# Kernel tuning notes

Measured on AMD Instinct MI355X. Metric: run time of the kernel, lower is better.

Reference implementation:

```python
import jax, jax.numpy as jnp
import numpy as np

N_MODELS = 16
IN_F = 1024
OUT_F = 1024
N_TOK = 8192


def setup_inputs() -> dict:
    key = jax.random.key(0)
    k1, k2, k3, k4 = jax.random.split(key, 4)
    x = jax.random.normal(k1, (N_TOK, IN_F), dtype=jnp.float32)
    idxs = jax.random.randint(k2, (N_TOK,), 0, N_MODELS, dtype=jnp.int64)
    w = jax.random.normal(k3, (N_MODELS, IN_F, OUT_F), dtype=jnp.float32) * 0.02
    b = jax.random.normal(k4, (N_MODELS, OUT_F), dtype=jnp.float32) * 0.02
    return {"x": x, "idxs": idxs, "w": w, "b": b}


def reference(x, idxs, w, b):
    # Equivalent math to the torch loop: for each expert i, tokens with
    # idxs==i get x @ w[i] + b[i]; finally ReLU over all outputs.
    # Loop over the small fixed expert count; selection by mask avoids
    # materializing the [N, E, out] tensor or gathering per-token weights.
    y = jnp.zeros((x.shape[0], w.shape[2]), dtype=x.dtype)
    for i in range(w.shape[0]):
        yi = x @ w[i] + b[i]  # [N, out]
        y = jnp.where((idxs == i)[:, None], yi, y)
    return jax.nn.relu(y)
```

## Files before the change

### kernel.cpp

```cpp
#include <hip/hip_runtime.h>
#include <hip/hip_bf16.h>
#include <stdint.h>

#define N_MODELS 16
#define IN_F 1024
#define OUT_F 1024
#define N_TOK 8192

#define BM 128
#define BN 128
#define BK 32
#define LDA 40

using us4   = __attribute__((ext_vector_type(4))) unsigned short;
using s16x8 = __attribute__((ext_vector_type(8))) short;
using f32x4 = __attribute__((ext_vector_type(4))) float;

__device__ __forceinline__ unsigned short f2bf(float f) {
    union { float f; uint32_t u; } v;
    v.f = f;
    uint32_t u = v.u;
    u += 0x7fffu + ((u >> 16) & 1u);
    return (unsigned short)(u >> 16);
}

__global__ void bucket_kernel(const int* __restrict__ idxs,
                              int* __restrict__ perm,
                              int* __restrict__ offs,
                              int* __restrict__ tile_off)
{
    __shared__ int cnt[N_MODELS];
    __shared__ int cur[N_MODELS];
    int t = threadIdx.x;
    if (t < N_MODELS) cnt[t] = 0;
    __syncthreads();
    for (int i = t; i < N_TOK; i += 256) atomicAdd(&cnt[idxs[i]], 1);
    __syncthreads();
    if (t == 0) {
        int o = 0, to = 0;
        for (int e = 0; e < N_MODELS; ++e) {
            offs[e] = o; tile_off[e] = to; cur[e] = o;
            to += (cnt[e] + BM - 1) / BM;
            o  += cnt[e];
        }
        offs[N_MODELS] = o; tile_off[N_MODELS] = to;
    }
    __syncthreads();
    for (int i = t; i < N_TOK; i += 256) {
        int e = idxs[i];
        int p = atomicAdd(&cur[e], 1);
        perm[p] = i;
    }
}

#define TT 64
__global__ void transpose_w_kernel(const float* __restrict__ w,
                                   unsigned short* __restrict__ wT)
{
    __shared__ unsigned short tile[TT][TT + 8];
    int e  = blockIdx.z;
    int n0 = blockIdx.y * TT;
    int k0 = blockIdx.x * TT;
    int t  = threadIdx.x;
    const float* wp = w + (size_t)e * IN_F * OUT_F;
    int c4 = (t & 15) * 4;
    int r  = t >> 4;
#pragma unroll
    for (int i = 0; i < 4; ++i) {
        int k = r + i * 16;
        const float4 v = *(const float4*)(wp + (size_t)(k0 + k) * OUT_F + n0 + c4);
        us4 pk;
        pk.x = f2bf(v.x); pk.y = f2bf(v.y); pk.z = f2bf(v.z); pk.w = f2bf(v.w);
        *(us4*)(&tile[k][c4]) = pk;
    }
    __syncthreads();
#pragma unroll
    for (int i = 0; i < 4; ++i) {
        int n = r + i * 16;
        us4 pk;
        pk.x = tile[c4 + 0][n];
        pk.y = tile[c4 + 1][n];
        pk.z = tile[c4 + 2][n];
        pk.w = tile[c4 + 3][n];
        *(us4*)(wT + (size_t)e * IN_F * OUT_F + (size_t)(n0 + n) * IN_F + k0 + c4) = pk;
    }
}

__global__ __launch_bounds__(256)
void gemm_kernel(const float* __restrict__ x,
                 const unsigned short* __restrict__ wT,
                 const float* __restrict__ bias,
                 const int* __restrict__ perm,
                 const int* __restrict__ offs,
                 const int* __restrict__ tile_off,
                 float* __restrict__ out)
{
    __shared__ unsigned short As[BM * LDA];
    __shared__ unsigned short Bs[BN * LDA];
    __shared__ int   permS[BM];
    __shared__ float biasS[BN];
    __shared__ int   toS[N_MODELS + 1];

    int t  = threadIdx.x;
    int bt = blockIdx.y;
    int n0 = blockIdx.x * BN;

    if (t <= N_MODELS) toS[t] = tile_off[t];
    __syncthreads();
    if (bt >= toS[N_MODELS]) return;

    int e = 0;
    while (toS[e + 1] <= bt) ++e;
    int mt_blk = bt - toS[e];
    int sBeg = offs[e];
    int sEnd = offs[e + 1];
    int s0 = sBeg + mt_blk * BM;
    int mValid = sEnd - s0; if (mValid > BM) mValid = BM;

    if (t < BM) permS[t] = (s0 + t < sEnd) ? perm[s0 + t] : 0;
    if (t < BN) biasS[t] = bias[(size_t)e * OUT_F + n0 + t];
    __syncthreads();

    const unsigned short* wTp = wT + (size_t)e * IN_F * OUT_F;

    f32x4 acc[4][4];
#pragma unroll
    for (int i = 0; i < 4; ++i)
#pragma unroll
        for (int j = 0; j < 4; ++j)
            acc[i][j] = (f32x4){0.f, 0.f, 0.f, 0.f};

    int lane = t & 63;
    int w    = t >> 6;
    int wm   = (w >> 1) * 64;
    int wn   = (w & 1) * 64;
    int m    = lane & 15;
    int q    = lane >> 4;

    int ar   = t >> 3;
    int apos = t & 7;
    int br   = t >> 2;
    int bpos = t & 3;

    for (int k0 = 0; k0 < IN_F; k0 += BK) {
#pragma unroll
        for (int i = 0; i < 4; ++i) {
            int r = ar + i * 32;
            int tok = permS[r];
            const float4 v = *(const float4*)(x + (size_t)tok * IN_F + k0 + apos * 4);
            us4 pk;
            pk.x = f2bf(v.x); pk.y = f2bf(v.y); pk.z = f2bf(v.z); pk.w = f2bf(v.w);
            *(us4*)(&As[r * LDA + apos * 4]) = pk;
        }
#pragma unroll
        for (int i = 0; i < 2; ++i) {
            int r = br + i * 64;
            s16x8 v = *(const s16x8*)(wTp + (size_t)(n0 + r) * IN_F + k0 + bpos * 8);
            *(s16x8*)(&Bs[r * LDA + bpos * 8]) = v;
        }
        __syncthreads();

        s16x8 af[4], bfr[4];
#pragma unroll
        for (int mt = 0; mt < 4; ++mt)
            af[mt] = *(const s16x8*)(&As[(wm + mt * 16 + m) * LDA + q * 8]);
#pragma unroll
        for (int nt = 0; nt < 4; ++nt)
            bfr[nt] = *(const s16x8*)(&Bs[(wn + nt * 16 + m) * LDA + q * 8]);
#pragma unroll
        for (int mt = 0; mt < 4; ++mt)
#pragma unroll
            for (int nt = 0; nt < 4; ++nt)
                acc[mt][nt] = __builtin_amdgcn_mfma_f32_16x16x32_bf16(
                    af[mt], bfr[nt], acc[mt][nt], 0, 0, 0);
        __syncthreads();
    }

#pragma unroll
    for (int mt = 0; mt < 4; ++mt) {
        int rbase = wm + mt * 16 + q * 4;
#pragma unroll
        for (int i = 0; i < 4; ++i) {
            int r = rbase + i;
            if (r < mValid) {
                int tok = permS[r];
                float* orow = out + (size_t)tok * OUT_F + n0;
#pragma unroll
                for (int nt = 0; nt < 4; ++nt) {
                    int c = wn + nt * 16 + m;
                    float v = acc[mt][nt][i] + biasS[c];
                    orow[c] = v > 0.f ? v : 0.f;
                }
            }
        }
    }
}

extern "C" void kernel_launch(void* const* d_in, const int* in_sizes, int n_in,
                              void* d_out, int out_size, void* d_ws, size_t ws_size,
                              hipStream_t stream) {
    const float* x    = (const float*)d_in[0];
    const int*   idxs = (const int*)d_in[1];
    const float* w    = (const float*)d_in[2];
    const float* b    = (const float*)d_in[3];
    float* out = (float*)d_out;

    unsigned short* wT = (unsigned short*)d_ws;
    int* perm     = (int*)((char*)d_ws + (size_t)N_MODELS * IN_F * OUT_F * sizeof(unsigned short));
    int* offs     = perm + N_TOK;
    int* tile_off = offs + (N_MODELS + 1);

    bucket_kernel<<<1, 256, 0, stream>>>(idxs, perm, offs, tile_off);
    transpose_w_kernel<<<dim3(IN_F / TT, OUT_F / TT, N_MODELS), 256, 0, stream>>>(w, wT);
    gemm_kernel<<<dim3(OUT_F / BN, 80), 256, 0, stream>>>(x, wT, b, perm, offs, tile_off, out);
}
```

Measured before the change: 209.6 us.

## Pre-pack gathered x and weights into MFMA-ready tiles, load via global_load_lds

A merged prep kernel converts the weights to bf16 and writes them in a tile-blocked, fragment-ordered layout. The same kernel gathers and converts the routed token rows of x into a per-tile packed bf16 buffer. The GEMM then streams contiguous 8 KB chunks straight into LDS with global_load_lds and does no conversion or gather work inside its k-loop. This removes per-iteration fp32 conversion and scattered row loads from the GEMM, at the cost of an extra write and read of the packed x buffer and more workspace.

Result: faster. 194.5 us (-7.2%).

```diff
diff --git a/kernel.cpp b/kernel.cpp
--- a/kernel.cpp
+++ b/kernel.cpp
@@ -6,22 +6,25 @@
 #define IN_F 1024
 #define OUT_F 1024
 #define N_TOK 8192
-
-#define BM 128
-#define BN 128
-#define BK 32
-#define LDA 40
-
+#define MAX_MT 80
+
+typedef unsigned short u16;
 using us4   = __attribute__((ext_vector_type(4))) unsigned short;
 using s16x8 = __attribute__((ext_vector_type(8))) short;
 using f32x4 = __attribute__((ext_vector_type(4))) float;
 
-__device__ __forceinline__ unsigned short f2bf(float f) {
+__device__ __forceinline__ u16 f2bf(float f) {
     union { float f; uint32_t u; } v;
     v.f = f;
     uint32_t u = v.u;
     u += 0x7fffu + ((u >> 16) & 1u);
-    return (unsigned short)(u >> 16);
+    return (u16)(u >> 16);
+}
+
+__device__ __forceinline__ void gload16(const u16* g, u16* l) {
+    __builtin_amdgcn_global_load_lds(
+        (const __attribute__((address_space(1))) void*)g,
+        (__attribute__((address_space(3))) void*)l, 16, 0, 0);
 }
 
 __global__ void bucket_kernel(const int* __restrict__ idxs,
@@ -40,7 +43,7 @@
         int o = 0, to = 0;
         for (int e = 0; e < N_MODELS; ++e) {
             offs[e] = o; tile_off[e] = to; cur[e] = o;
-            to += (cnt[e] + BM - 1) / BM;
+            to += (cnt[e] + 127) / 128;
             o  += cnt[e];
         }
         offs[N_MODELS] = o; tile_off[N_MODELS] = to;
@@ -53,57 +56,105 @@
     }
 }
 
-#define TT 64
-__global__ void transpose_w_kernel(const float* __restrict__ w,
-                                   unsigned short* __restrict__ wT)
+#define WBLOCKS (16*8*16)
+#define SH_S 132
+
+__global__ __launch_bounds__(256)
+void prep_kernel(const float* __restrict__ w, const float* __restrict__ x,
+                 const int* __restrict__ perm, const int* __restrict__ offs,
+                 const int* __restrict__ tile_off,
+                 u16* __restrict__ wT, u16* __restrict__ xg)
 {
-    __shared__ unsigned short tile[TT][TT + 8];
-    int e  = blockIdx.z;
-    int n0 = blockIdx.y * TT;
-    int k0 = blockIdx.x * TT;
+    __shared__ u16 sh[64 * SH_S];
     int t  = threadIdx.x;
-    const float* wp = w + (size_t)e * IN_F * OUT_F;
-    int c4 = (t & 15) * 4;
-    int r  = t >> 4;
-#pragma unroll
-    for (int i = 0; i < 4; ++i) {
-        int k = r + i * 16;
-        const float4 v = *(const float4*)(wp + (size_t)(k0 + k) * OUT_F + n0 + c4);
-        us4 pk;
-        pk.x = f2bf(v.x); pk.y = f2bf(v.y); pk.z = f2bf(v.z); pk.w = f2bf(v.w);
-        *(us4*)(&tile[k][c4]) = pk;
-    }
-    __syncthreads();
-#pragma unroll
-    for (int i = 0; i < 4; ++i) {
-        int n = r + i * 16;
-        us4 pk;
-        pk.x = tile[c4 + 0][n];
-        pk.y = tile[c4 + 1][n];
-        pk.z = tile[c4 + 2][n];
-        pk.w = tile[c4 + 3][n];
-        *(us4*)(wT + (size_t)e * IN_F * OUT_F + (size_t)(n0 + n) * IN_F + k0 + c4) = pk;
+    int bx = blockIdx.x;
+
+    if (bx < WBLOCKS) {
+        int e  = bx >> 7;
+        int nt = (bx >> 4) & 7;
+        int kg = bx & 15;
+        const float* wp = w + (size_t)e * 1048576 + (size_t)kg * 65536 + nt * 128;
+        int n4  = t & 31;
+        int kr0 = t >> 5;
+#pragma unroll
+        for (int p = 0; p < 8; ++p) {
+            int kr = kr0 + p * 8;
+            const float4 v = *(const float4*)(wp + (size_t)kr * 1024 + n4 * 4);
+            us4 pk; pk.x = f2bf(v.x); pk.y = f2bf(v.y); pk.z = f2bf(v.z); pk.w = f2bf(v.w);
+            *(us4*)(&sh[kr * SH_S + n4 * 4]) = pk;
+        }
+        __syncthreads();
+        int n  = t & 127;
+        int qh = t >> 7;
+        u16* outb = wT + ((size_t)(e * 8 + nt) * 32) * 4096;
+#pragma unroll
+        for (int oct = 0; oct < 4; ++oct) {
+            int ko = qh + oct * 2;
+            int kb = kg * 2 + (ko >> 2);
+            int q  = ko & 3;
+            s16x8 v;
+#pragma unroll
+            for (int j = 0; j < 8; ++j) v[j] = (short)sh[(ko * 8 + j) * SH_S + n];
+            *(s16x8*)(outb + ((size_t)kb * 4 + q) * 1024 + n * 8) = v;
+        }
+    } else {
+        int bx2 = bx - WBLOCKS;
+        int mt = bx2 >> 3;
+        int kg = bx2 & 7;
+        int total = tile_off[16];
+        if (mt >= total) return;
+        int e = 0;
+        while (tile_off[e + 1] <= mt) ++e;
+        int s0   = offs[e] + (mt - tile_off[e]) * 128;
+        int sEnd = offs[e + 1];
+        int r0   = t >> 3;
+        int apos = t & 7;
+        int toks[4];
+#pragma unroll
+        for (int i = 0; i < 4; ++i) {
+            int r = r0 + i * 32;
+            toks[i] = (s0 + r < sEnd) ? perm[s0 + r] : -1;
+        }
+        u16* outx = xg + (size_t)mt * 32 * 4096;
+        for (int kb4 = 0; kb4 < 4; ++kb4) {
+            int kb = kg * 4 + kb4;
+#pragma unroll
+            for (int i = 0; i < 4; ++i) {
+                int r = r0 + i * 32;
+                int k = kb * 32 + apos * 4;
+                float4 v;
+                if (toks[i] >= 0) v = *(const float4*)(x + (size_t)toks[i] * 1024 + k);
+                else              v = make_float4(0.f, 0.f, 0.f, 0.f);
+                us4 pk; pk.x = f2bf(v.x); pk.y = f2bf(v.y); pk.z = f2bf(v.z); pk.w = f2bf(v.w);
+                *(us4*)(&sh[(apos >> 1) * 1024 + r * 8 + (apos & 1) * 4]) = pk;
+            }
+            __syncthreads();
+#pragma unroll
+            for (int i = 0; i < 2; ++i) {
+                int c = t + i * 256;
+                *(s16x8*)(outx + (size_t)kb * 4096 + c * 8) = *(const s16x8*)(&sh[c * 8]);
+            }
+            __syncthreads();
+        }
     }
 }
 
 __global__ __launch_bounds__(256)
-void gemm_kernel(const float* __restrict__ x,
-                 const unsigned short* __restrict__ wT,
+void gemm_kernel(const u16* __restrict__ xg, const u16* __restrict__ wT,
                  const float* __restrict__ bias,
-                 const int* __restrict__ perm,
-                 const int* __restrict__ offs,
+                 const int* __restrict__ perm, const int* __restrict__ offs,
                  const int* __restrict__ tile_off,
                  float* __restrict__ out)
 {
-    __shared__ unsigned short As[BM * LDA];
-    __shared__ unsigned short Bs[BN * LDA];
-    __shared__ int   permS[BM];
-    __shared__ float biasS[BN];
+    __shared__ u16 As[4096];
+    __shared__ u16 Bs[4096];
+    __shared__ int   permS[128];
+    __shared__ float biasS[128];
     __shared__ int   toS[N_MODELS + 1];
 
     int t  = threadIdx.x;
     int bt = blockIdx.y;
-    int n0 = blockIdx.x * BN;
+    int nt = blockIdx.x;
 
     if (t <= N_MODELS) toS[t] = tile_off[t];
     __syncthreads();
@@ -111,17 +162,24 @@
 
     int e = 0;
     while (toS[e + 1] <= bt) ++e;
-    int mt_blk = bt - toS[e];
-    int sBeg = offs[e];
+    int s0   = offs[e] + (bt - toS[e]) * 128;
     int sEnd = offs[e + 1];
-    int s0 = sBeg + mt_blk * BM;
-    int mValid = sEnd - s0; if (mValid > BM) mValid = BM;
-
-    if (t < BM) permS[t] = (s0 + t < sEnd) ? perm[s0 + t] : 0;
-    if (t < BN) biasS[t] = bias[(size_t)e * OUT_F + n0 + t];
-    __syncthreads();
-
-    const unsigned short* wTp = wT + (size_t)e * IN_F * OUT_F;
+    int mValid = sEnd - s0; if (mValid > 128) mValid = 128;
+
+    if (t < 128) {
+        permS[t] = (s0 + t < sEnd) ? perm[s0 + t] : 0;
+        biasS[t] = bias[(size_t)e * OUT_F + nt * 128 + t];
+    }
+
+    const u16* atile = xg + (size_t)bt * 32 * 4096;
+    const u16* btile = wT + ((size_t)(e * 8 + nt) * 32) * 4096;
+
+    int lane = t & 63;
+    int wv   = t >> 6;
+    int wm   = (wv >> 1) * 64;
+    int wn   = (wv & 1) * 64;
+    int m    = lane & 15;
+    int q    = lane >> 4;
 
     f32x4 acc[4][4];
 #pragma unroll
@@ -130,66 +188,47 @@
         for (int j = 0; j < 4; ++j)
             acc[i][j] = (f32x4){0.f, 0.f, 0.f, 0.f};
 
-    int lane = t & 63;
-    int w    = t >> 6;
-    int wm   = (w >> 1) * 64;
-    int wn   = (w & 1) * 64;
-    int m    = lane & 15;
-    int q    = lane >> 4;
-
-    int ar   = t >> 3;
-    int apos = t & 7;
-    int br   = t >> 2;
-    int bpos = t & 3;
-
-    for (int k0 = 0; k0 < IN_F; k0 += BK) {
-#pragma unroll
-        for (int i = 0; i < 4; ++i) {
-            int r = ar + i * 32;
-            int tok = permS[r];
-            const float4 v = *(const float4*)(x + (size_t)tok * IN_F + k0 + apos * 4);
-            us4 pk;
-            pk.x = f2bf(v.x); pk.y = f2bf(v.y); pk.z = f2bf(v.z); pk.w = f2bf(v.w);
-            *(us4*)(&As[r * LDA + apos * 4]) = pk;
-        }
-#pragma unroll
-        for (int i = 0; i < 2; ++i) {
-            int r = br + i * 64;
-            s16x8 v = *(const s16x8*)(wTp + (size_t)(n0 + r) * IN_F + k0 + bpos * 8);
-            *(s16x8*)(&Bs[r * LDA + bpos * 8]) = v;
-        }
+    int c = wv * 2;
+
+    for (int kb = 0; kb < 32; ++kb) {
+        const u16* ga = atile + kb * 4096;
+        const u16* gb = btile + kb * 4096;
+        gload16(ga + (c    ) * 512 + lane * 8, &As[(c    ) * 512]);
+        gload16(ga + (c + 1) * 512 + lane * 8, &As[(c + 1) * 512]);
+        gload16(gb + (c    ) * 512 + lane * 8, &Bs[(c    ) * 512]);
+        gload16(gb + (c + 1) * 512 + lane * 8, &Bs[(c + 1) * 512]);
         __syncthreads();
 
-        s16x8 af[4], bfr[4];
-#pragma unroll
-        for (int mt = 0; mt < 4; ++mt)
-            af[mt] = *(const s16x8*)(&As[(wm + mt * 16 + m) * LDA + q * 8]);
-#pragma unroll
-        for (int nt = 0; nt < 4; ++nt)
-            bfr[nt] = *(const s16x8*)(&Bs[(wn + nt * 16 + m) * LDA + q * 8]);
-#pragma unroll
-        for (int mt = 0; mt < 4; ++mt)
-#pragma unroll
-            for (int nt = 0; nt < 4; ++nt)
-                acc[mt][nt] = __builtin_amdgcn_mfma_f32_16x16x32_bf16(
-                    af[mt], bfr[nt], acc[mt][nt], 0, 0, 0);
+        s16x8 af[4], bf[4];
+#pragma unroll
+        for (int mt2 = 0; mt2 < 4; ++mt2)
+            af[mt2] = *(const s16x8*)(&As[q * 1024 + (wm + mt2 * 16 + m) * 8]);
+#pragma unroll
+        for (int nt2 = 0; nt2 < 4; ++nt2)
+            bf[nt2] = *(const s16x8*)(&Bs[q * 1024 + (wn + nt2 * 16 + m) * 8]);
+#pragma unroll
+        for (int mt2 = 0; mt2 < 4; ++mt2)
+#pragma unroll
+            for (int nt2 = 0; nt2 < 4; ++nt2)
+                acc[mt2][nt2] = __builtin_amdgcn_mfma_f32_16x16x32_bf16(
+                    af[mt2], bf[nt2], acc[mt2][nt2], 0, 0, 0);
         __syncthreads();
     }
 
 #pragma unroll
-    for (int mt = 0; mt < 4; ++mt) {
-        int rbase = wm + mt * 16 + q * 4;
+    for (int mt2 = 0; mt2 < 4; ++mt2) {
+        int rbase = wm + mt2 * 16 + q * 4;
 #pragma unroll
         for (int i = 0; i < 4; ++i) {
             int r = rbase + i;
             if (r < mValid) {
                 int tok = permS[r];
-                float* orow = out + (size_t)tok * OUT_F + n0;
-#pragma unroll
-                for (int nt = 0; nt < 4; ++nt) {
-                    int c = wn + nt * 16 + m;
-                    float v = acc[mt][nt][i] + biasS[c];
-                    orow[c] = v > 0.f ? v : 0.f;
+                float* orow = out + (size_t)tok * OUT_F + nt * 128;
+#pragma unroll
+                for (int nt2 = 0; nt2 < 4; ++nt2) {
+                    int col = wn + nt2 * 16 + m;
+                    float v = acc[mt2][nt2][i] + biasS[col];
+                    orow[col] = v > 0.f ? v : 0.f;
                 }
             }
         }
@@ -205,12 +244,13 @@
     const float* b    = (const float*)d_in[3];
     float* out = (float*)d_out;
 
-    unsigned short* wT = (unsigned short*)d_ws;
-    int* perm     = (int*)((char*)d_ws + (size_t)N_MODELS * IN_F * OUT_F * sizeof(unsigned short));
+    u16* wT = (u16*)d_ws;
+    u16* xg = wT + (size_t)N_MODELS * IN_F * OUT_F;
+    int* perm     = (int*)(xg + (size_t)MAX_MT * 32 * 4096);
     int* offs     = perm + N_TOK;
     int* tile_off = offs + (N_MODELS + 1);
 
     bucket_kernel<<<1, 256, 0, stream>>>(idxs, perm, offs, tile_off);
-    transpose_w_kernel<<<dim3(IN_F / TT, OUT_F / TT, N_MODELS), 256, 0, stream>>>(w, wT);
-    gemm_kernel<<<dim3(OUT_F / BN, 80), 256, 0, stream>>>(x, wT, b, perm, offs, tile_off, out);
-}
+    prep_kernel<<<WBLOCKS + 640, 256, 0, stream>>>(w, x, perm, offs, tile_off, wT, xg);
+    gemm_kernel<<<dim3(8, MAX_MT), 256, 0, stream>>>(xg, wT, b, perm, offs, tile_off, out);
+}
```
